# Kernel tuning notes

Measured on AMD Instinct MI355X. Metric: run time of the kernel, lower is better.

The kernel has to match this reference:

```python
import jax, jax.numpy as jnp
import numpy as np

N_NODES = 100000
D = 64


def setup_inputs() -> dict:
    key = jax.random.key(0)
    ks = jax.random.split(key, 8)
    x = jax.random.normal(ks[0], (N_NODES, D), dtype=jnp.float32)
    edge_index = jax.random.randint(ks[1], (2, 1000000), 0, N_NODES, dtype=jnp.int64)
    s = 1.0 / np.sqrt(D)
    W0 = jax.random.uniform(ks[2], (D, D), jnp.float32, -s, s)
    W1 = jax.random.uniform(ks[3], (D, D), jnp.float32, -s, s)
    W2 = jax.random.uniform(ks[4], (D, D), jnp.float32, -s, s)
    b0 = jnp.zeros((D,), jnp.float32)
    b1 = jnp.zeros((D,), jnp.float32)
    b2 = jnp.zeros((D,), jnp.float32)
    return {"x": x, "edge_index": edge_index,
            "W0": W0, "b0": b0, "W1": W1, "b1": b1, "W2": W2, "b2": b2}


def _gcn_layer(x, src, dst, norm, W, b):
    # GCNConv: h = D^{-1/2}(A+I)D^{-1/2} (x W) + b
    h = x @ W                                   # [N, D_out]
    msg = h[src] * norm[:, None]                # gather + scale, [E', D_out]
    agg = jax.ops.segment_sum(msg, dst, num_segments=x.shape[0])
    return jax.nn.relu(agg + b)


def reference(x, edge_index, W0, b0, W1, b1, W2, b2):
    n = x.shape[0]
    # add self loops (GCNConv default add_self_loops=True)
    loops = jnp.arange(n, dtype=edge_index.dtype)
    src = jnp.concatenate([edge_index[0], loops])
    dst = jnp.concatenate([edge_index[1], loops])
    # symmetric normalization deg^{-1/2}[src] * deg^{-1/2}[dst]
    deg = jax.ops.segment_sum(jnp.ones_like(src, dtype=x.dtype), dst, num_segments=n)
    dinv = jnp.where(deg > 0, jax.lax.rsqrt(deg), 0.0)
    norm = dinv[src] * dinv[dst]                # [E']
    # dropout p=0.0 / eval mode -> identity
    h = _gcn_layer(x, src, dst, norm, W0, b0)
    h = _gcn_layer(h, src, dst, norm, W1, b1)
    h = _gcn_layer(h, src, dst, norm, W2, b2)
    return h
```

## Files before the change

kernel.cpp:

```cpp
#include <hip/hip_runtime.h>
#include <hip/hip_fp16.h>

#define N_NODES 100000
#define CAP 64
#define NB  391
#define BE  2048

typedef _Float16 v4h __attribute__((ext_vector_type(4)));
typedef float    v4f __attribute__((ext_vector_type(4)));


__global__ __launch_bounds__(256) void k_bucket(
    const int* __restrict__ src, const int* __restrict__ dst, int E, int NBLK,
    unsigned int* __restrict__ arr, unsigned short* __restrict__ scantab,
    const float* __restrict__ W0, const float* __restrict__ W1,
    const float* __restrict__ W2,
    __half* __restrict__ Wt0h, __half* __restrict__ Wt0l,
    __half* __restrict__ Wt1, __half* __restrict__ Wt2) {
    if ((int)blockIdx.x == NBLK) {
        for (int i = threadIdx.x; i < 4096; i += 256) {
            int k = i >> 6, c = i & 63;
            float w0 = W0[i];
            __half w0h = __float2half(w0);
            Wt0h[(c << 6) + k] = w0h;
            Wt0l[(c << 6) + k] = __float2half(w0 - __half2float(w0h));
            Wt1[(c << 6) + k] = __float2half(W1[i]);
            Wt2[(c << 6) + k] = __float2half(W2[i]);
        }
        return;
    }
    __shared__ int cnt[392];
    __shared__ int scn[392];
    __shared__ int gsum[98];
    int t = threadIdx.x;
    for (int j = t; j < 392; j += 256) cnt[j] = 0;
    __syncthreads();
    int blk = blockIdx.x;
    int base = blk * BE;
    int dsts[8], rnk[8];
#pragma unroll
    for (int i = 0; i < 8; i++) {
        int e = base + i * 256 + t;
        int d = (e < E) ? dst[e] : -1;
        dsts[i] = d;
        rnk[i] = (d >= 0) ? atomicAdd(&cnt[d >> 8], 1) : 0;
    }
    __syncthreads();
    if (t < 98) gsum[t] = cnt[4 * t] + cnt[4 * t + 1] + cnt[4 * t + 2] + cnt[4 * t + 3];
    __syncthreads();
    if (t == 0) {
        int run = 0;
#pragma unroll 1
        for (int g = 0; g < 98; g++) { int c = gsum[g]; gsum[g] = run; run += c; }
    }
    __syncthreads();
    if (t < 98) {
        int b0 = gsum[t];
        int c0 = cnt[4 * t], c1 = cnt[4 * t + 1], c2 = cnt[4 * t + 2];
        scn[4 * t]     = b0;
        scn[4 * t + 1] = b0 + c0;
        scn[4 * t + 2] = b0 + c0 + c1;
        scn[4 * t + 3] = b0 + c0 + c1 + c2;
    }
    __syncthreads();
#pragma unroll
    for (int i = 0; i < 8; i++) {
        int d = dsts[i];
        if (d >= 0) {
            int e = base + i * 256 + t;
            int s = src[e];
            int pos = scn[d >> 8] + rnk[i];
            arr[(size_t)blk * BE + pos] =
                ((unsigned)(d & 255) << 17) | (unsigned)s;
        }
    }
    for (int j = t; j < 392; j += 256)
        scantab[(size_t)blk * 392 + j] = (unsigned short)scn[j];
}

__global__ __launch_bounds__(256) void k_build(
    const unsigned int* __restrict__ arr,
    const unsigned short* __restrict__ scantab,
    int* __restrict__ csr, int* __restrict__ deg, int NBLK, int n) {
    __shared__ int cnt[256];
    int t = threadIdx.x;
    cnt[t] = 0;
    __syncthreads();
    int b = blockIdx.x;
    int bn = b << 8;
    for (int blk = t; blk < NBLK; blk += 256) {
        int s0 = scantab[(size_t)blk * 392 + b];
        int s1 = scantab[(size_t)blk * 392 + b + 1];
        const unsigned int* a = arr + (size_t)blk * BE;
        for (int k = s0; k < s1; k++) {
            unsigned v = a[k];
            int dloc = (int)(v >> 17);
            int sv = (int)(v & 0x1FFFF);
            int r = atomicAdd(&cnt[dloc], 1);
            if (r < CAP) csr[((bn + dloc) << 6) + r] = sv;
        }
    }
    __syncthreads();
    int nd = bn + t;
    if (nd < n) deg[nd] = cnt[t];
}

__global__ __launch_bounds__(256) void k_gemm0(const float* __restrict__ x,
                                               const __half* __restrict__ Wth,
                                               const __half* __restrict__ Wtl,
                                               const int* __restrict__ deg,
                                               __half* __restrict__ outh) {
    __shared__ _Float16 xs_hi[16 * 68];
    __shared__ _Float16 xs_lo[16 * 68];
    __shared__ float dsv[16];
    int t = threadIdx.x;
    int rl = t >> 4, q = t & 15;
    int lane = t & 63;
    int w = t >> 6;
    int col = (w << 4) + (lane & 15);
    int g = lane >> 4;
    int node = blockIdx.x * 16 + rl;

    v4f xv = __builtin_nontemporal_load((const v4f*)x + (size_t)blockIdx.x * 256 + t);
    int dg = deg[node];
    float d_i = rsqrtf((float)(dg + 1));
    if (q == 0) dsv[rl] = d_i;

    const v4h* wth4 = (const v4h*)(Wth + ((size_t)col << 6));
    const v4h* wtl4 = (const v4h*)(Wtl + ((size_t)col << 6));
    v4h bfh[4], bfl[4];
#pragma unroll
    for (int s = 0; s < 4; s++) { bfh[s] = wth4[(s << 2) + g]; bfl[s] = wtl4[(s << 2) + g]; }

    v4h yh = {(_Float16)xv.x, (_Float16)xv.y, (_Float16)xv.z, (_Float16)xv.w};
    v4h yl = {(_Float16)(xv.x - (float)yh.x), (_Float16)(xv.y - (float)yh.y),
              (_Float16)(xv.z - (float)yh.z), (_Float16)(xv.w - (float)yh.w)};
    *(v4h*)&xs_hi[rl * 68 + (q << 2)] = yh;
    *(v4h*)&xs_lo[rl * 68 + (q << 2)] = yl;
    __syncthreads();

    v4f acc = {0.f, 0.f, 0.f, 0.f};
    int arow = lane & 15;
#pragma unroll
    for (int s = 0; s < 4; s++) {
        v4h al = *(const v4h*)&xs_lo[arow * 68 + (s << 4) + (g << 2)];
        v4h ah = *(const v4h*)&xs_hi[arow * 68 + (s << 4) + (g << 2)];
        acc = __builtin_amdgcn_mfma_f32_16x16x16f16(al, bfh[s], acc, 0, 0, 0);
        acc = __builtin_amdgcn_mfma_f32_16x16x16f16(ah, bfl[s], acc, 0, 0, 0);
        acc = __builtin_amdgcn_mfma_f32_16x16x16f16(ah, bfh[s], acc, 0, 0, 0);
    }
#pragma unroll
    for (int j = 0; j < 4; j++) {
        int r = (g << 2) + j;
        float v = acc[j] * dsv[r];
        outh[((size_t)(blockIdx.x * 16 + r) << 6) + col] = __float2half(v);
    }
}


__device__ __forceinline__ uint4 padd4(uint4 u, uint4 v) {
    __half2* a = (__half2*)&u;
    __half2* b = (__half2*)&v;
    uint4 r;
    __half2* c = (__half2*)&r;
#pragma unroll
    for (int k = 0; k < 4; k++) c[k] = __hadd2(a[k], b[k]);
    return r;
}

__device__ __forceinline__ void acc_h4(v4f& A, v4f& B, uint4 v) {
    __half2* h = (__half2*)&v;
    float2 f0 = __half22float2(h[0]);
    float2 f1 = __half22float2(h[1]);
    float2 f2 = __half22float2(h[2]);
    float2 f3 = __half22float2(h[3]);
    v4f fa = {f0.x, f0.y, f1.x, f1.y};
    v4f fb = {f2.x, f2.y, f3.x, f3.y};
    A = A + fa;
    B = B + fb;
}

__device__ __forceinline__ void gather_acc4(const uint4* __restrict__ h4,
                                            const int* __restrict__ csr,
                                            int4 ia, int4 ib,
                                            int node, int qq, int cnt,
                                            v4f& yA, v4f& yB) {
    const int4* c4 = (const int4*)(csr + (node << 6));
    v4f A0 = {0,0,0,0}, A1 = {0,0,0,0}, A2 = {0,0,0,0}, A3 = {0,0,0,0};
    v4f B0 = {0,0,0,0}, B1 = {0,0,0,0}, B2 = {0,0,0,0}, B3 = {0,0,0,0};
    acc_h4(A0, B0, h4[(size_t)node * 8 + qq]);
    int e = 0;
    for (; e + 8 <= cnt; ) {
        uint4 v0 = h4[(size_t)ia.x * 8 + qq];
        uint4 v1 = h4[(size_t)ia.y * 8 + qq];
        uint4 v2 = h4[(size_t)ia.z * 8 + qq];
        uint4 v3 = h4[(size_t)ia.w * 8 + qq];
        uint4 v4 = h4[(size_t)ib.x * 8 + qq];
        uint4 v5 = h4[(size_t)ib.y * 8 + qq];
        uint4 v6 = h4[(size_t)ib.z * 8 + qq];
        uint4 v7 = h4[(size_t)ib.w * 8 + qq];
        e += 8;
        ia = c4[e >> 2];
        ib = c4[(e >> 2) + 1];
        uint4 p0 = padd4(v0, v1);
        uint4 p1 = padd4(v2, v3);
        uint4 p2 = padd4(v4, v5);
        uint4 p3 = padd4(v6, v7);
        acc_h4(A0, B0, p0); acc_h4(A1, B1, p1);
        acc_h4(A2, B2, p2); acc_h4(A3, B3, p3);
    }
    if (e + 4 <= cnt) {
        uint4 v0 = h4[(size_t)ia.x * 8 + qq];
        uint4 v1 = h4[(size_t)ia.y * 8 + qq];
        uint4 v2 = h4[(size_t)ia.z * 8 + qq];
        uint4 v3 = h4[(size_t)ia.w * 8 + qq];
        uint4 p0 = padd4(v0, v1);
        uint4 p1 = padd4(v2, v3);
        acc_h4(A1, B1, p0); acc_h4(A2, B2, p1);
        e += 4;
        ia = ib;
    }
    int rem = cnt - e;
    if (rem > 0) {
        int j0 = ia.x;
        int j1 = (rem > 1) ? ia.y : j0;
        int j2 = (rem > 2) ? ia.z : j0;
        uint4 v0 = h4[(size_t)j0 * 8 + qq];
        uint4 v1 = h4[(size_t)j1 * 8 + qq];
        uint4 v2 = h4[(size_t)j2 * 8 + qq];
        acc_h4(A1, B1, v0);
        if (rem > 1) acc_h4(A2, B2, v1);
        if (rem > 2) acc_h4(A3, B3, v2);
    }
    yA = (A0 + A1) + (A2 + A3);
    yB = (B0 + B1) + (B2 + B3);
}

__global__ __launch_bounds__(256) void k_gather_gemm(const uint4* __restrict__ h4,
                                                     const int* __restrict__ csr,
                                                     const int* __restrict__ deg,
                                                     const float* __restrict__ bias,
                                                     const __half* __restrict__ Wt,
                                                     __half* __restrict__ outh, int n) {
    __shared__ _Float16 xs_hi[32 * 68];
    __shared__ _Float16 xs_lo[32 * 68];
    __shared__ float dsv[32];
    (void)n;
    int t = threadIdx.x;
    int nl = t >> 3, qq = t & 7;
    int node = blockIdx.x * 32 + nl;
    int lane = t & 63;
    int w = t >> 6;
    int col = (w << 4) + (lane & 15);
    int g = lane >> 4;

    const int4* c4 = (const int4*)(csr + (node << 6));
    int4 ia0 = c4[0];
    int4 ib0 = c4[1];
    int dg = deg[node];
    int cnt = min(dg, CAP);
    float d_i = rsqrtf((float)(dg + 1));
    if (qq == 0) dsv[nl] = d_i;
    float4 bA = ((const float4*)bias)[qq * 2 + 0];
    float4 bB = ((const float4*)bias)[qq * 2 + 1];

    v4f aA, aB;
    gather_acc4(h4, csr, ia0, ib0, node, qq, cnt, aA, aB);

    const v4h* wt4 = (const v4h*)(Wt + ((size_t)col << 6));
    v4h bf[4];
#pragma unroll
    for (int s = 0; s < 4; s++) bf[s] = wt4[(s << 2) + g];

    float y0 = fmaxf(fmaf(aA.x, d_i, bA.x), 0.f);
    float y1 = fmaxf(fmaf(aA.y, d_i, bA.y), 0.f);
    float y2 = fmaxf(fmaf(aA.z, d_i, bA.z), 0.f);
    float y3 = fmaxf(fmaf(aA.w, d_i, bA.w), 0.f);
    float y4 = fmaxf(fmaf(aB.x, d_i, bB.x), 0.f);
    float y5 = fmaxf(fmaf(aB.y, d_i, bB.y), 0.f);
    float y6 = fmaxf(fmaf(aB.z, d_i, bB.z), 0.f);
    float y7 = fmaxf(fmaf(aB.w, d_i, bB.w), 0.f);
    v4h yhA = {(_Float16)y0, (_Float16)y1, (_Float16)y2, (_Float16)y3};
    v4h ylA = {(_Float16)(y0 - (float)yhA.x), (_Float16)(y1 - (float)yhA.y),
               (_Float16)(y2 - (float)yhA.z), (_Float16)(y3 - (float)yhA.w)};
    v4h yhB = {(_Float16)y4, (_Float16)y5, (_Float16)y6, (_Float16)y7};
    v4h ylB = {(_Float16)(y4 - (float)yhB.x), (_Float16)(y5 - (float)yhB.y),
               (_Float16)(y6 - (float)yhB.z), (_Float16)(y7 - (float)yhB.w)};
    *(v4h*)&xs_hi[nl * 68 + (qq << 3) + 0] = yhA;
    *(v4h*)&xs_hi[nl * 68 + (qq << 3) + 4] = yhB;
    *(v4h*)&xs_lo[nl * 68 + (qq << 3) + 0] = ylA;
    *(v4h*)&xs_lo[nl * 68 + (qq << 3) + 4] = ylB;
    __syncthreads();

    v4f acc0 = {0.f, 0.f, 0.f, 0.f};
    v4f acc1 = {0.f, 0.f, 0.f, 0.f};
    int ar = lane & 15;
#pragma unroll
    for (int s = 0; s < 4; s++) {
        int ko = (s << 4) + (g << 2);
        v4h al0 = *(const v4h*)&xs_lo[ar * 68 + ko];
        v4h ah0 = *(const v4h*)&xs_hi[ar * 68 + ko];
        v4h al1 = *(const v4h*)&xs_lo[(ar + 16) * 68 + ko];
        v4h ah1 = *(const v4h*)&xs_hi[(ar + 16) * 68 + ko];
        acc0 = __builtin_amdgcn_mfma_f32_16x16x16f16(al0, bf[s], acc0, 0, 0, 0);
        acc0 = __builtin_amdgcn_mfma_f32_16x16x16f16(ah0, bf[s], acc0, 0, 0, 0);
        acc1 = __builtin_amdgcn_mfma_f32_16x16x16f16(al1, bf[s], acc1, 0, 0, 0);
        acc1 = __builtin_amdgcn_mfma_f32_16x16x16f16(ah1, bf[s], acc1, 0, 0, 0);
    }

#pragma unroll
    for (int j = 0; j < 4; j++) {
        int r0 = (g << 2) + j;
        float v0 = acc0[j] * dsv[r0];
        outh[((size_t)(blockIdx.x * 32 + r0) << 6) + col] = __float2half(v0);
        int r1 = r0 + 16;
        float v1 = acc1[j] * dsv[r1];
        outh[((size_t)(blockIdx.x * 32 + r1) << 6) + col] = __float2half(v1);
    }
}

__global__ __launch_bounds__(256) void k_gather(const uint4* __restrict__ h4,
                                                const int* __restrict__ csr,
                                                const int* __restrict__ deg,
                                                const float* __restrict__ bias,
                                                float* __restrict__ out, int n) {
    int t = threadIdx.x;
    int nl = t >> 3, qq = t & 7;
    int node = blockIdx.x * 32 + nl;
    if (node >= n) return;
    const int4* c4 = (const int4*)(csr + (node << 6));
    int4 ia0 = c4[0];
    int4 ib0 = c4[1];
    int dg = deg[node];
    int cnt = min(dg, CAP);
    float d = rsqrtf((float)(dg + 1));
    v4f aA, aB;
    gather_acc4(h4, csr, ia0, ib0, node, qq, cnt, aA, aB);
    float4 bA = ((const float4*)bias)[qq * 2 + 0];
    float4 bB = ((const float4*)bias)[qq * 2 + 1];
    float4 rA, rB;
    rA.x = fmaxf(fmaf(aA.x, d, bA.x), 0.f);
    rA.y = fmaxf(fmaf(aA.y, d, bA.y), 0.f);
    rA.z = fmaxf(fmaf(aA.z, d, bA.z), 0.f);
    rA.w = fmaxf(fmaf(aA.w, d, bA.w), 0.f);
    rB.x = fmaxf(fmaf(aB.x, d, bB.x), 0.f);
    rB.y = fmaxf(fmaf(aB.y, d, bB.y), 0.f);
    rB.z = fmaxf(fmaf(aB.z, d, bB.z), 0.f);
    rB.w = fmaxf(fmaf(aB.w, d, bB.w), 0.f);
    ((float4*)out)[(size_t)node * 16 + qq * 2 + 0] = rA;
    ((float4*)out)[(size_t)node * 16 + qq * 2 + 1] = rB;
}


extern "C" void kernel_launch(void* const* d_in, const int* in_sizes, int n_in,
                              void* d_out, int out_size, void* d_ws, size_t ws_size,
                              hipStream_t stream) {
    const float* x  = (const float*)d_in[0];
    const int*   ei = (const int*)d_in[1];
    const float* W0 = (const float*)d_in[2];
    const float* b0 = (const float*)d_in[3];
    const float* W1 = (const float*)d_in[4];
    const float* b1 = (const float*)d_in[5];
    const float* W2 = (const float*)d_in[6];
    const float* b2 = (const float*)d_in[7];
    float* out = (float*)d_out;

    const int N = N_NODES;
    int E = in_sizes[1] / 2;
    const int* src = ei;
    const int* dst = ei + E;
    const int NBLK = (E + BE - 1) / BE;

    char* p = (char*)d_ws;
    auto alloc = [&](size_t bytes) -> void* {
        void* r = (void*)p;
        p += (bytes + 511) & ~(size_t)511;
        return r;
    };
    int*    deg  = (int*)alloc((size_t)N * 4);
    unsigned int*   arr     = (unsigned int*)alloc((size_t)NBLK * BE * 4);
    unsigned short* scantab = (unsigned short*)alloc((size_t)NBLK * 392 * 2);
    int*    csr  = (int*)alloc((size_t)N * CAP * 4);
    uint4*  hA   = (uint4*)alloc((size_t)N * 64 * 2);
    uint4*  hB   = (uint4*)alloc((size_t)N * 64 * 2);
    __half* Wt0h = (__half*)alloc(4096 * 2);
    __half* Wt0l = (__half*)alloc(4096 * 2);
    __half* Wt1  = (__half*)alloc(4096 * 2);
    __half* Wt2  = (__half*)alloc(4096 * 2);

    const int GEMM_B = N / 16;
    const int GATH_B = N / 32;

    k_bucket<<<NBLK + 1, 256, 0, stream>>>(src, dst, E, NBLK, arr, scantab,
                                           W0, W1, W2, Wt0h, Wt0l, Wt1, Wt2);
    k_build<<<NB, 256, 0, stream>>>(arr, scantab, csr, deg, NBLK, N);
    k_gemm0<<<GEMM_B, 256, 0, stream>>>(x, Wt0h, Wt0l, deg, (__half*)hA);
    k_gather_gemm<<<GATH_B, 256, 0, stream>>>(hA, csr, deg, b0, Wt1, (__half*)hB, N);
    k_gather_gemm<<<GATH_B, 256, 0, stream>>>(hB, csr, deg, b1, Wt2, (__half*)hA, N);
    k_gather<<<GATH_B, 256, 0, stream>>>(hA, csr, deg, b2, out, N);
}
```

Baseline: 232.7 us.

## Fuse CSR build with first-layer GEMM and stage CSR rows in LDS

Merges the CSR build and the layer-0 GEMM into one kernel, so each build block runs the x@W0 tiles for its 256 nodes using the degrees already in shared memory. This removes a launch and the global read of deg. CSR rows are now assembled in a 64KB LDS buffer and written out with coalesced int4 stores instead of scattered global writes. The bucket kernel also loads src early and replaces the serial 98-element prefix scan with a parallel Hillis-Steele scan. In exchange the GEMM work shrinks from 6250 blocks to 391 blocks that loop over 16 tiles each, and the large LDS footprint lowers occupancy.

```diff
diff --git a/kernel.cpp b/kernel.cpp
--- a/kernel.cpp
+++ b/kernel.cpp
@@ -31,32 +31,37 @@
     }
     __shared__ int cnt[392];
     __shared__ int scn[392];
-    __shared__ int gsum[98];
+    __shared__ int gs[98];
     int t = threadIdx.x;
     for (int j = t; j < 392; j += 256) cnt[j] = 0;
     __syncthreads();
     int blk = blockIdx.x;
     int base = blk * BE;
-    int dsts[8], rnk[8];
+    int dsts[8], srcs[8], rnk[8];
 #pragma unroll
     for (int i = 0; i < 8; i++) {
         int e = base + i * 256 + t;
         int d = (e < E) ? dst[e] : -1;
+        srcs[i] = (e < E) ? src[e] : 0;
         dsts[i] = d;
         rnk[i] = (d >= 0) ? atomicAdd(&cnt[d >> 8], 1) : 0;
     }
     __syncthreads();
-    if (t < 98) gsum[t] = cnt[4 * t] + cnt[4 * t + 1] + cnt[4 * t + 2] + cnt[4 * t + 3];
-    __syncthreads();
-    if (t == 0) {
-        int run = 0;
-#pragma unroll 1
-        for (int g = 0; g < 98; g++) { int c = gsum[g]; gsum[g] = run; run += c; }
-    }
-    __syncthreads();
+    int c0 = 0, c1 = 0, c2 = 0, c3 = 0;
     if (t < 98) {
-        int b0 = gsum[t];
-        int c0 = cnt[4 * t], c1 = cnt[4 * t + 1], c2 = cnt[4 * t + 2];
+        c0 = cnt[4 * t]; c1 = cnt[4 * t + 1]; c2 = cnt[4 * t + 2]; c3 = cnt[4 * t + 3];
+        gs[t] = c0 + c1 + c2 + c3;
+    }
+    __syncthreads();
+#pragma unroll
+    for (int off = 1; off < 128; off <<= 1) {
+        int u = (t < 98 && t >= off) ? gs[t - off] : 0;
+        __syncthreads();
+        if (t < 98) gs[t] += u;
+        __syncthreads();
+    }
+    if (t < 98) {
+        int b0 = gs[t] - (c0 + c1 + c2 + c3);
         scn[4 * t]     = b0;
         scn[4 * t + 1] = b0 + c0;
         scn[4 * t + 2] = b0 + c0 + c1;
@@ -67,22 +72,27 @@
     for (int i = 0; i < 8; i++) {
         int d = dsts[i];
         if (d >= 0) {
-            int e = base + i * 256 + t;
-            int s = src[e];
             int pos = scn[d >> 8] + rnk[i];
             arr[(size_t)blk * BE + pos] =
-                ((unsigned)(d & 255) << 17) | (unsigned)s;
+                ((unsigned)(d & 255) << 17) | (unsigned)srcs[i];
         }
     }
     for (int j = t; j < 392; j += 256)
         scantab[(size_t)blk * 392 + j] = (unsigned short)scn[j];
 }
 
-__global__ __launch_bounds__(256) void k_build(
+__global__ __launch_bounds__(256) void k_build0(
     const unsigned int* __restrict__ arr,
     const unsigned short* __restrict__ scantab,
-    int* __restrict__ csr, int* __restrict__ deg, int NBLK, int n) {
+    int* __restrict__ csr, int* __restrict__ deg, int NBLK, int n,
+    const float* __restrict__ x,
+    const __half* __restrict__ Wth, const __half* __restrict__ Wtl,
+    __half* __restrict__ outh) {
+    __shared__ int4 lcsr4[4096];
     __shared__ int cnt[256];
+    __shared__ _Float16 xs_hi[16 * 68];
+    __shared__ _Float16 xs_lo[16 * 68];
+    int* lcsr = (int*)lcsr4;
     int t = threadIdx.x;
     cnt[t] = 0;
     __syncthreads();
@@ -97,63 +107,55 @@
             int dloc = (int)(v >> 17);
             int sv = (int)(v & 0x1FFFF);
             int r = atomicAdd(&cnt[dloc], 1);
-            if (r < CAP) csr[((bn + dloc) << 6) + r] = sv;
+            if (r < CAP) lcsr[(dloc << 6) + r] = sv;
         }
     }
     __syncthreads();
-    int nd = bn + t;
-    if (nd < n) deg[nd] = cnt[t];
-}
-
-__global__ __launch_bounds__(256) void k_gemm0(const float* __restrict__ x,
-                                               const __half* __restrict__ Wth,
-                                               const __half* __restrict__ Wtl,
-                                               const int* __restrict__ deg,
-                                               __half* __restrict__ outh) {
-    __shared__ _Float16 xs_hi[16 * 68];
-    __shared__ _Float16 xs_lo[16 * 68];
-    __shared__ float dsv[16];
-    int t = threadIdx.x;
+    int rows = min(256, n - bn);
+    int4* cdst = (int4*)(csr + ((size_t)bn << 6));
+    for (int i = t; i < rows * 16; i += 256) cdst[i] = lcsr4[i];
+    if (bn + t < n) deg[bn + t] = cnt[t];
     int rl = t >> 4, q = t & 15;
     int lane = t & 63;
     int w = t >> 6;
     int col = (w << 4) + (lane & 15);
     int g = lane >> 4;
-    int node = blockIdx.x * 16 + rl;
-
-    v4f xv = __builtin_nontemporal_load((const v4f*)x + (size_t)blockIdx.x * 256 + t);
-    int dg = deg[node];
-    float d_i = rsqrtf((float)(dg + 1));
-    if (q == 0) dsv[rl] = d_i;
-
     const v4h* wth4 = (const v4h*)(Wth + ((size_t)col << 6));
     const v4h* wtl4 = (const v4h*)(Wtl + ((size_t)col << 6));
     v4h bfh[4], bfl[4];
 #pragma unroll
     for (int s = 0; s < 4; s++) { bfh[s] = wth4[(s << 2) + g]; bfl[s] = wtl4[(s << 2) + g]; }
 
-    v4h yh = {(_Float16)xv.x, (_Float16)xv.y, (_Float16)xv.z, (_Float16)xv.w};
-    v4h yl = {(_Float16)(xv.x - (float)yh.x), (_Float16)(xv.y - (float)yh.y),
-              (_Float16)(xv.z - (float)yh.z), (_Float16)(xv.w - (float)yh.w)};
-    *(v4h*)&xs_hi[rl * 68 + (q << 2)] = yh;
-    *(v4h*)&xs_lo[rl * 68 + (q << 2)] = yl;
-    __syncthreads();
-
-    v4f acc = {0.f, 0.f, 0.f, 0.f};
-    int arow = lane & 15;
-#pragma unroll
-    for (int s = 0; s < 4; s++) {
-        v4h al = *(const v4h*)&xs_lo[arow * 68 + (s << 4) + (g << 2)];
-        v4h ah = *(const v4h*)&xs_hi[arow * 68 + (s << 4) + (g << 2)];
-        acc = __builtin_amdgcn_mfma_f32_16x16x16f16(al, bfh[s], acc, 0, 0, 0);
-        acc = __builtin_amdgcn_mfma_f32_16x16x16f16(ah, bfl[s], acc, 0, 0, 0);
-        acc = __builtin_amdgcn_mfma_f32_16x16x16f16(ah, bfh[s], acc, 0, 0, 0);
-    }
-#pragma unroll
-    for (int j = 0; j < 4; j++) {
-        int r = (g << 2) + j;
-        float v = acc[j] * dsv[r];
-        outh[((size_t)(blockIdx.x * 16 + r) << 6) + col] = __float2half(v);
+    int tiles = rows >> 4;
+    for (int it = 0; it < tiles; it++) {
+        int nb16 = bn + it * 16;
+        v4f xv = __builtin_nontemporal_load((const v4f*)x + (size_t)nb16 * 16 + t);
+        float d_i = rsqrtf((float)(cnt[it * 16 + rl] + 1));
+        v4h yh = {(_Float16)xv.x, (_Float16)xv.y, (_Float16)xv.z, (_Float16)xv.w};
+        v4h yl = {(_Float16)(xv.x - (float)yh.x), (_Float16)(xv.y - (float)yh.y),
+                  (_Float16)(xv.z - (float)yh.z), (_Float16)(xv.w - (float)yh.w)};
+        (void)d_i;
+        *(v4h*)&xs_hi[rl * 68 + (q << 2)] = yh;
+        *(v4h*)&xs_lo[rl * 68 + (q << 2)] = yl;
+        __syncthreads();
+        v4f acc = {0.f, 0.f, 0.f, 0.f};
+        int arow = lane & 15;
+#pragma unroll
+        for (int s = 0; s < 4; s++) {
+            v4h al = *(const v4h*)&xs_lo[arow * 68 + (s << 4) + (g << 2)];
+            v4h ah = *(const v4h*)&xs_hi[arow * 68 + (s << 4) + (g << 2)];
+            acc = __builtin_amdgcn_mfma_f32_16x16x16f16(al, bfh[s], acc, 0, 0, 0);
+            acc = __builtin_amdgcn_mfma_f32_16x16x16f16(ah, bfl[s], acc, 0, 0, 0);
+            acc = __builtin_amdgcn_mfma_f32_16x16x16f16(ah, bfh[s], acc, 0, 0, 0);
+        }
+#pragma unroll
+        for (int j = 0; j < 4; j++) {
+            int r = (g << 2) + j;
+            float dr = rsqrtf((float)(cnt[it * 16 + r] + 1));
+            float v = acc[j] * dr;
+            outh[((size_t)(nb16 + r) << 6) + col] = __float2half(v);
+        }
+        __syncthreads();
     }
 }
 
@@ -388,13 +390,12 @@
     __half* Wt1  = (__half*)alloc(4096 * 2);
     __half* Wt2  = (__half*)alloc(4096 * 2);
 
-    const int GEMM_B = N / 16;
     const int GATH_B = N / 32;
 
     k_bucket<<<NBLK + 1, 256, 0, stream>>>(src, dst, E, NBLK, arr, scantab,
                                            W0, W1, W2, Wt0h, Wt0l, Wt1, Wt2);
-    k_build<<<NB, 256, 0, stream>>>(arr, scantab, csr, deg, NBLK, N);
-    k_gemm0<<<GEMM_B, 256, 0, stream>>>(x, Wt0h, Wt0l, deg, (__half*)hA);
+    k_build0<<<NB, 256, 0, stream>>>(arr, scantab, csr, deg, NBLK, N,
+                                     x, Wt0h, Wt0l, (__half*)hA);
     k_gather_gemm<<<GATH_B, 256, 0, stream>>>(hA, csr, deg, b0, Wt1, (__half*)hB, N);
     k_gather_gemm<<<GATH_B, 256, 0, stream>>>(hB, csr, deg, b1, Wt2, (__half*)hA, N);
     k_gather<<<GATH_B, 256, 0, stream>>>(hA, csr, deg, b2, out, N);
```

Result: faster. 219.4 us (-5.7%).
